# Performance work log

Hardware: AMD Instinct MI355X
Metric: run time of the kernel (lower is better)

The kernel has to match this reference:

```python
import jax, jax.numpy as jnp
import numpy as np

N_NODES = 100000
N_EDGES = 3200000
N_GRAPHS = 512
IN_DIM, HID, OUT, N_CLS = 32, 64, 64, 10


def _linear_params(key, din, dout, scale=0.05):
    k1, k2 = jax.random.split(key)
    return (jax.random.normal(k1, (din, dout), jnp.float32) * scale,
            jax.random.normal(k2, (dout,), jnp.float32) * scale)


def setup_inputs() -> dict:
    key = jax.random.key(0)
    ks = jax.random.split(key, 12)
    x = jax.random.normal(ks[0], (N_NODES, IN_DIM), jnp.float32)
    edge_index = jax.random.randint(ks[1], (2, N_EDGES), 0, N_NODES, jnp.int64)
    batch = jnp.sort(jax.random.randint(ks[2], (N_NODES,), 0, N_GRAPHS, jnp.int64))
    W_emb, b_emb = _linear_params(ks[3], IN_DIM, HID)
    W1, b1 = _linear_params(ks[4], HID, HID)
    W2, b2 = _linear_params(ks[5], HID, HID)
    W3, b3 = _linear_params(ks[6], HID, HID)
    W4, b4 = _linear_params(ks[7], HID, OUT)
    Wr1, br1 = _linear_params(ks[8], OUT, OUT // 2)
    Wr2, br2 = _linear_params(ks[9], OUT // 2, OUT // 4)
    Wr3, br3 = _linear_params(ks[10], OUT // 4, N_CLS)
    return dict(x=x, edge_index=edge_index, batch=batch, n_graphs=N_GRAPHS,
                W_emb=W_emb, b_emb=b_emb, W1=W1, b1=b1, W2=W2, b2=b2,
                W3=W3, b3=b3, W4=W4, b4=b4, Wr1=Wr1, br1=br1,
                Wr2=Wr2, br2=br2, Wr3=Wr3, br3=br3)


def reference(x, edge_index, batch, n_graphs,
              W_emb, b_emb, W1, b1, W2, b2, W3, b3, W4, b4,
              Wr1, br1, Wr2, br2, Wr3, br3):
    n = x.shape[0]
    # PyG GCNConv(normalize=True): add self-loops, symmetric D^{-1/2} norm
    self_idx = jnp.arange(n, dtype=edge_index.dtype)
    src = jnp.concatenate([edge_index[0], self_idx])  # [E+N]
    dst = jnp.concatenate([edge_index[1], self_idx])
    deg = jax.ops.segment_sum(jnp.ones(src.shape[0], x.dtype), dst, num_segments=n)
    dis = jnp.where(deg > 0, jax.lax.rsqrt(deg), 0.0)
    norm = dis[src] * dis[dst]  # [E+N]

    def gcn_conv(h, W, b):
        h = h @ W                              # [N, D]
        msg = h[src] * norm[:, None]           # gather + scale, [E+N, D]
        agg = jax.ops.segment_sum(msg, dst, num_segments=n)  # scatter-add
        return agg + b

    h = x @ W_emb + b_emb
    h = jax.nn.relu(gcn_conv(h, W1, b1))
    h = jax.nn.relu(gcn_conv(h, W2, b2))
    h = jax.nn.relu(gcn_conv(h, W3, b3))
    h = jax.nn.relu(gcn_conv(h, W4, b4))

    # global mean pool over graphs
    sums = jax.ops.segment_sum(h, batch, num_segments=n_graphs)
    cnts = jax.ops.segment_sum(jnp.ones(n, h.dtype), batch, num_segments=n_graphs)
    pooled = sums / jnp.maximum(cnts, 1.0)[:, None]

    r = jax.nn.relu(pooled @ Wr1 + br1)
    r = jax.nn.relu(r @ Wr2 + br2)
    logits = r @ Wr3 + br3
    return jax.nn.log_softmax(logits, axis=1)
```

## Files before the change

kernel.cpp:

```cpp
#include <hip/hip_runtime.h>
#include <hip/hip_bf16.h>

typedef __hip_bfloat16 bf16;
typedef short bf16x8 __attribute__((ext_vector_type(8)));
typedef float f32x4 __attribute__((ext_vector_type(4)));

#define N_NODES 100000
#define N_EDGES 3200000
#define N_GRAPHS 512
#define NBKT    ((N_NODES + 255) / 256)
#define CAP     10496
#define EPB     16384
#define NBLK_A  ((N_EDGES + EPB - 1) / EPB)
#define FP4_SCALE 16.0f
#define FP4_INV   (1.0f / 16.0f)


__device__ inline float fp8_to_f32(unsigned int b) {
    unsigned s = (b >> 7) & 1, e = (b >> 3) & 15, m = b & 7;
    float v = (e == 0) ? (float)m * 0.001953125f
                       : __uint_as_float(((e + 120u) << 23) | (m << 20));
    return s ? -v : v;
}

__device__ inline void acc4(float* a, unsigned v) {
#if __has_builtin(__builtin_amdgcn_cvt_pk_f32_fp8)
    typedef float f32x2 __attribute__((ext_vector_type(2)));
    f32x2 lo = __builtin_amdgcn_cvt_pk_f32_fp8((int)v, false);
    f32x2 hi = __builtin_amdgcn_cvt_pk_f32_fp8((int)v, true);
    a[0] += lo.x; a[1] += lo.y; a[2] += hi.x; a[3] += hi.y;
#elif __has_builtin(__builtin_amdgcn_cvt_f32_fp8)
    a[0] += __builtin_amdgcn_cvt_f32_fp8(v, 0);
    a[1] += __builtin_amdgcn_cvt_f32_fp8(v, 1);
    a[2] += __builtin_amdgcn_cvt_f32_fp8(v, 2);
    a[3] += __builtin_amdgcn_cvt_f32_fp8(v, 3);
#else
    a[0] += fp8_to_f32(v & 0xFF);
    a[1] += fp8_to_f32((v >> 8) & 0xFF);
    a[2] += fp8_to_f32((v >> 16) & 0xFF);
    a[3] += fp8_to_f32((v >> 24) & 0xFF);
#endif
}


__device__ inline void accf4(float* a, float* b, unsigned d) {
#if __has_builtin(__builtin_amdgcn_perm)
    unsigned lo8 = __builtin_amdgcn_perm(0x4C484440u, 0x3C383000u, d & 0x07070707u)
                 | ((d & 0x08080808u) << 4);
    unsigned hi8 = __builtin_amdgcn_perm(0x4C484440u, 0x3C383000u, (d >> 4) & 0x07070707u)
                 | (d & 0x80808080u);
#else
    unsigned lo8 = 0, hi8 = 0;
    #pragma unroll
    for (int i = 0; i < 4; ++i) {
        unsigned ln = (d >> (8 * i)) & 7u, hs_ = (d >> (8 * i)) & 0x80u;
        unsigned hn = (d >> (8 * i + 4)) & 7u, ls_ = ((d >> (8 * i)) & 8u) << 4;
        unsigned lb = (ln < 2) ? ln * 0x30u : (0x30u + (ln << 2));
        unsigned hb = (hn < 2) ? hn * 0x30u : (0x30u + (hn << 2));
        lo8 |= (lb | ls_) << (8 * i);
        hi8 |= (hb | hs_) << (8 * i);
    }
#endif
    acc4(a, lo8);
    acc4(b, hi8);
}


__device__ inline unsigned fp4n(float v) {
    unsigned s = (__float_as_uint(v) >> 28) & 8u;
    float x = fabsf(v);
    unsigned n = (unsigned)(x >= 0.25f) + (x >= 0.75f) + (x >= 1.25f) + (x >= 1.75f)
               + (x >= 2.5f) + (x >= 3.5f) + (x >= 5.0f);
    return s | n;
}

__device__ inline unsigned short f2bf(float x) {
    unsigned u = __float_as_uint(x);
    return (unsigned short)((u + 0x7FFF + ((u >> 16) & 1)) >> 16);
}


__global__ void k_setup(const float* __restrict__ W_emb, const float* __restrict__ b_emb,
                        const float* __restrict__ W1, const float* __restrict__ W2,
                        const float* __restrict__ W3, const float* __restrict__ W4,
                        float* __restrict__ Wc, float* __restrict__ bc,
                        unsigned short* __restrict__ Wfrag, int* __restrict__ gcur,
                        unsigned* __restrict__ ta, unsigned* __restrict__ tb) {
    int blk = blockIdx.x, t = threadIdx.x;
    if (blk == 0) {
        for (int i = t; i < 32 * 64; i += 256) {
            int a = i / 64, b = i % 64;
            float acc = 0.f;
            for (int k = 0; k < 64; ++k) acc += W_emb[a * 64 + k] * W1[k * 64 + b];
            Wc[i] = acc;
        }
        if (t < 64) {
            float acc = 0.f;
            for (int k = 0; k < 64; ++k) acc += b_emb[k] * W1[k * 64 + t];
            bc[t] = acc;
        }
    } else if (blk <= 3) {
        const float* W = (blk == 1) ? W2 : (blk == 2) ? W3 : W4;
        unsigned short* dst = Wfrag + (size_t)(blk - 1) * 4096;
        for (int i = 0; i < 16; ++i) {
            int flat = t * 16 + i;
            int j = flat & 7, lane = (flat >> 3) & 63, mt = (flat >> 9) & 3, kt = flat >> 11;
            int m = mt * 16 + (lane & 15);
            int k = kt * 32 + ((lane >> 4) << 3) + j;
            dst[flat] = f2bf(W[k * 64 + m]);
        }
    } else {
        for (int b = t; b < NBKT; b += 256) gcur[b] = b * CAP;
        if (t < 8) {
            size_t o = (size_t)N_NODES * 8 + t;
            ta[o] = 0; tb[o] = 0;
        }
    }
}


__global__ void __launch_bounds__(512) k_bucket(const int* __restrict__ ei,
                                                int* __restrict__ gcur,
                                                int* __restrict__ ebuf) {
    __shared__ int cnt[NBKT];
    __shared__ int base[NBKT];
    int t = threadIdx.x;
    for (int i = t; i < NBKT; i += 512) cnt[i] = 0;
    __syncthreads();
    int e0 = blockIdx.x * EPB + t;
    int sv[32], dv[32];
    #pragma unroll
    for (int j = 0; j < 32; ++j) {
        int e = e0 + j * 512;
        if (e < N_EDGES) {
            sv[j] = ei[e];
            dv[j] = ei[N_EDGES + e];
            atomicAdd(&cnt[dv[j] >> 8], 1);
        } else dv[j] = -1;
    }
    __syncthreads();
    for (int i = t; i < NBKT; i += 512) {
        base[i] = atomicAdd(&gcur[i], cnt[i]);
        cnt[i] = 0;
    }
    __syncthreads();
    #pragma unroll
    for (int j = 0; j < 32; ++j) {
        if (dv[j] >= 0) {
            int b = dv[j] >> 8;
            int r = atomicAdd(&cnt[b], 1);
            ebuf[base[b] + r] = (sv[j] << 8) | (dv[j] & 255);
        }
    }
}


__global__ void __launch_bounds__(256) k_fill2(const int* __restrict__ ebuf,
                                               const int* __restrict__ gcur,
                                               int2* __restrict__ rc,
                                               float* __restrict__ dis,
                                               int* __restrict__ col) {
    __shared__ int cnt[256];
    __shared__ int sc[256];
    __shared__ int exs[256];
    __shared__ int cur[256];
    int b = blockIdx.x, t = threadIdx.x;
    int n0 = b * 256;
    int nrec = gcur[b] - b * CAP;
    const int* eb = ebuf + (size_t)b * CAP;
    int* cw = col + (size_t)b * CAP;
    cnt[t] = 0; cur[t] = 0;
    __syncthreads();
    for (int i = t; i < nrec; i += 256)
        atomicAdd(&cnt[eb[i] & 255], 1);
    __syncthreads();
    int c0 = cnt[t];
    int a8 = (c0 + 7) & ~7;
    sc[t] = a8; __syncthreads();
    for (int off = 1; off < 256; off <<= 1) {
        int u = (t >= off) ? sc[t - off] : 0;
        __syncthreads();
        sc[t] += u;
        __syncthreads();
    }
    int myex = sc[t] - a8;
    exs[t] = myex;
    int n = n0 + t;
    if (n < N_NODES) {
        rc[n] = make_int2(b * CAP + myex, c0);
        dis[n] = rsqrtf((float)(c0 + 1));
    }
    for (int i = myex + c0; i < myex + a8; ++i) cw[i] = N_NODES;
    __syncthreads();
    for (int i = t; i < nrec; i += 256) {
        int rec = eb[i];
        int dl = rec & 255;
        cw[exs[dl] + atomicAdd(&cur[dl], 1)] = rec >> 8;
    }
}


__global__ void __launch_bounds__(256) k_mm1(const float* __restrict__ inp,
                                             const float* __restrict__ W,
                                             const float* __restrict__ bias,
                                             const float* __restrict__ dis,
                                             unsigned char* __restrict__ T) {
    __shared__ float Wl[32][64];
    __shared__ float hs[16][32];
    int t = threadIdx.x;
    for (int i = t; i < 32 * 64; i += 256) Wl[i / 64][i % 64] = W[i];
    int row0 = blockIdx.x * 16;
    for (int i = t; i < 16 * 32; i += 256) {
        int r = row0 + i / 32, k = i % 32;
        hs[i / 32][k] = inp[(size_t)r * 32 + k];
    }
    __syncthreads();
    int c = t & 63, rg = t >> 6;
    float a0 = 0, a1 = 0, a2 = 0, a3 = 0;
    #pragma unroll 4
    for (int k = 0; k < 32; ++k) {
        float wv = Wl[k][c];
        a0 += hs[rg * 4 + 0][k] * wv;
        a1 += hs[rg * 4 + 1][k] * wv;
        a2 += hs[rg * 4 + 2][k] * wv;
        a3 += hs[rg * 4 + 3][k] * wv;
    }
    float bv = bias[c];
    int r = row0 + rg * 4;
    unsigned n0 = fp4n(FP4_SCALE * dis[r + 0] * (a0 + bv));
    unsigned n1 = fp4n(FP4_SCALE * dis[r + 1] * (a1 + bv));
    unsigned n2 = fp4n(FP4_SCALE * dis[r + 2] * (a2 + bv));
    unsigned n3 = fp4n(FP4_SCALE * dis[r + 3] * (a3 + bv));
    unsigned p0 = __shfl_xor(n0, 1), p1 = __shfl_xor(n1, 1);
    unsigned p2 = __shfl_xor(n2, 1), p3 = __shfl_xor(n3, 1);
    if ((c & 1) == 0) {
        size_t boff = (size_t)(c >> 1);
        T[(size_t)(r + 0) * 32 + boff] = (unsigned char)(n0 | (p0 << 4));
        T[(size_t)(r + 1) * 32 + boff] = (unsigned char)(n1 | (p1 << 4));
        T[(size_t)(r + 2) * 32 + boff] = (unsigned char)(n2 | (p2 << 4));
        T[(size_t)(r + 3) * 32 + boff] = (unsigned char)(n3 | (p3 << 4));
    }
}


__global__ void __launch_bounds__(256, 8) k_agg(const unsigned* __restrict__ tph,
                                                const int2* __restrict__ rc,
                                                const int* __restrict__ col,
                                                unsigned short* __restrict__ agg) {
    int row = blockIdx.x * 32 + (threadIdx.x >> 3);
    int sl = threadIdx.x & 7;
    float a[4] = {0.f, 0.f, 0.f, 0.f};
    float b[4] = {0.f, 0.f, 0.f, 0.f};
    accf4(a, b, tph[(size_t)row * 8 + sl]);
    int2 r = rc[row];
    int nit = (r.y + 7) >> 3;
    const int* cp = col + r.x;
    if (nit > 0) {
        int4 c0 = *(const int4*)(cp + 0);
        int4 c1 = *(const int4*)(cp + 4);
        for (int it = 1; it < nit; ++it) {
            unsigned v0 = tph[(size_t)c0.x * 8 + sl];
            unsigned v1 = tph[(size_t)c0.y * 8 + sl];
            unsigned v2 = tph[(size_t)c0.z * 8 + sl];
            unsigned v3 = tph[(size_t)c0.w * 8 + sl];
            unsigned v4 = tph[(size_t)c1.x * 8 + sl];
            unsigned v5 = tph[(size_t)c1.y * 8 + sl];
            unsigned v6 = tph[(size_t)c1.z * 8 + sl];
            unsigned v7 = tph[(size_t)c1.w * 8 + sl];
            const int* np = cp + it * 8;
            c0 = *(const int4*)(np + 0);
            c1 = *(const int4*)(np + 4);
            accf4(a, b, v0); accf4(a, b, v1); accf4(a, b, v2); accf4(a, b, v3);
            accf4(a, b, v4); accf4(a, b, v5); accf4(a, b, v6); accf4(a, b, v7);
        }
        unsigned v0 = tph[(size_t)c0.x * 8 + sl];
        unsigned v1 = tph[(size_t)c0.y * 8 + sl];
        unsigned v2 = tph[(size_t)c0.z * 8 + sl];
        unsigned v3 = tph[(size_t)c0.w * 8 + sl];
        unsigned v4 = tph[(size_t)c1.x * 8 + sl];
        unsigned v5 = tph[(size_t)c1.y * 8 + sl];
        unsigned v6 = tph[(size_t)c1.z * 8 + sl];
        unsigned v7 = tph[(size_t)c1.w * 8 + sl];
        accf4(a, b, v0); accf4(a, b, v1); accf4(a, b, v2); accf4(a, b, v3);
        accf4(a, b, v4); accf4(a, b, v5); accf4(a, b, v6); accf4(a, b, v7);
    }
    uint4 o;
    o.x = (unsigned)f2bf(a[0]) | ((unsigned)f2bf(b[0]) << 16);
    o.y = (unsigned)f2bf(a[1]) | ((unsigned)f2bf(b[1]) << 16);
    o.z = (unsigned)f2bf(a[2]) | ((unsigned)f2bf(b[2]) << 16);
    o.w = (unsigned)f2bf(a[3]) | ((unsigned)f2bf(b[3]) << 16);
    *(uint4*)(agg + (size_t)row * 64 + sl * 8) = o;
}


__global__ void __launch_bounds__(256) k_combm(const unsigned short* __restrict__ agg,
                                               const float* __restrict__ dis,
                                               const float* __restrict__ bias,
                                               const unsigned short* __restrict__ Wfrag,
                                               unsigned char* __restrict__ T) {
    __shared__ unsigned short h_lds[64][72];
    int t = threadIdx.x;
    int rowbase = blockIdx.x * 64;
    {
        int row = t >> 2, q = t & 3;
        int grow = rowbase + row;
        if (grow < N_NODES) {
            float f = dis[grow] * FP4_INV;
            #pragma unroll
            for (int i = 0; i < 4; ++i) {
                int c0 = q * 16 + i * 4;
                ushort4 v = *(const ushort4*)(agg + (size_t)grow * 64 + c0);
                short4 o;
                o.x = (short)f2bf(fmaxf(f * __uint_as_float((unsigned)v.x << 16) + bias[c0 + 0], 0.f));
                o.y = (short)f2bf(fmaxf(f * __uint_as_float((unsigned)v.y << 16) + bias[c0 + 1], 0.f));
                o.z = (short)f2bf(fmaxf(f * __uint_as_float((unsigned)v.z << 16) + bias[c0 + 2], 0.f));
                o.w = (short)f2bf(fmaxf(f * __uint_as_float((unsigned)v.w << 16) + bias[c0 + 3], 0.f));
                *(short4*)&h_lds[row][c0] = o;
            }
        } else {
            #pragma unroll
            for (int i = 0; i < 4; ++i)
                *(short4*)&h_lds[row][q * 16 + i * 4] = make_short4(0, 0, 0, 0);
        }
    }
    __syncthreads();
    int w = t >> 6, l = t & 63;
    f32x4 acc[4] = {{0,0,0,0}, {0,0,0,0}, {0,0,0,0}, {0,0,0,0}};
    const bf16x8* wf = (const bf16x8*)Wfrag;
    #pragma unroll
    for (int kt = 0; kt < 2; ++kt) {
        bf16x8 bfr = *(const bf16x8*)&h_lds[w * 16 + (l & 15)][kt * 32 + ((l >> 4) << 3)];
        #pragma unroll
        for (int mt = 0; mt < 4; ++mt) {
            bf16x8 afr = wf[(kt * 4 + mt) * 64 + l];
            acc[mt] = __builtin_amdgcn_mfma_f32_16x16x32_bf16(afr, bfr, acc[mt], 0, 0, 0);
        }
    }
    int hrow = rowbase + w * 16 + (l & 15);
    if (hrow < N_NODES) {
        float sc2 = FP4_SCALE * dis[hrow];
        #pragma unroll
        for (int mt = 0; mt < 4; ++mt) {
            int colbase = mt * 16 + ((l >> 4) << 2);
            unsigned short v = (unsigned short)(fp4n(sc2 * acc[mt][0])
                               | (fp4n(sc2 * acc[mt][1]) << 4)
                               | (fp4n(sc2 * acc[mt][2]) << 8)
                               | (fp4n(sc2 * acc[mt][3]) << 12));
            *(unsigned short*)(T + (size_t)hrow * 32 + (colbase >> 1)) = v;
        }
    }
}


__global__ void __launch_bounds__(256) k_poolhead(const unsigned short* __restrict__ agg,
                                                  const float* __restrict__ dis,
                                                  const float* __restrict__ bias,
                                                  const int* __restrict__ batch,
                                                  const float* __restrict__ Wr1, const float* __restrict__ br1,
                                                  const float* __restrict__ Wr2, const float* __restrict__ br2,
                                                  const float* __restrict__ Wr3, const float* __restrict__ br3,
                                                  float* __restrict__ out) {
    __shared__ float part[4][64];
    __shared__ float p[64], r1[32], r2[16], lg[10];
    __shared__ int seg[2];
    int g = blockIdx.x, t = threadIdx.x;
    if (t < 2) {
        int key = g + t;
        int lo = 0, hi = N_NODES;
        while (lo < hi) { int m = (lo + hi) >> 1; if (batch[m] < key) lo = m + 1; else hi = m; }
        seg[t] = lo;
    }
    __syncthreads();
    int start = seg[0], end = seg[1];
    int w = t >> 6, grp = (t >> 4) & 3, sl = t & 15;
    float b0 = bias[sl * 4 + 0], b1 = bias[sl * 4 + 1];
    float b2 = bias[sl * 4 + 2], b3 = bias[sl * 4 + 3];
    float a[4] = {0.f, 0.f, 0.f, 0.f};
    for (int r = start + w * 4 + grp; r < end; r += 16) {
        ushort4 v = *(const ushort4*)(agg + (size_t)r * 64 + sl * 4);
        float s = dis[r] * FP4_INV;
        a[0] += fmaxf(s * __uint_as_float((unsigned)v.x << 16) + b0, 0.f);
        a[1] += fmaxf(s * __uint_as_float((unsigned)v.y << 16) + b1, 0.f);
        a[2] += fmaxf(s * __uint_as_float((unsigned)v.z << 16) + b2, 0.f);
        a[3] += fmaxf(s * __uint_as_float((unsigned)v.w << 16) + b3, 0.f);
    }
    #pragma unroll
    for (int j = 0; j < 4; ++j) {
        a[j] += __shfl_xor(a[j], 16);
        a[j] += __shfl_xor(a[j], 32);
    }
    if (sl == (t & 63)) {
        #pragma unroll
        for (int j = 0; j < 4; ++j) part[w][sl * 4 + j] = a[j];
    }
    __syncthreads();
    if (t < 64) {
        float s = part[0][t] + part[1][t] + part[2][t] + part[3][t];
        float c = fmaxf((float)(end - start), 1.f);
        p[t] = s / c;
    }
    __syncthreads();
    if (t < 32) {
        float acc = br1[t];
        for (int k = 0; k < 64; ++k) acc += p[k] * Wr1[k * 32 + t];
        r1[t] = fmaxf(acc, 0.f);
    }
    __syncthreads();
    if (t < 16) {
        float acc = br2[t];
        for (int k = 0; k < 32; ++k) acc += r1[k] * Wr2[k * 16 + t];
        r2[t] = fmaxf(acc, 0.f);
    }
    __syncthreads();
    if (t < 10) {
        float acc = br3[t];
        for (int k = 0; k < 16; ++k) acc += r2[k] * Wr3[k * 10 + t];
        lg[t] = acc;
    }
    __syncthreads();
    if (t < 10) {
        float m = -1e30f;
        for (int j = 0; j < 10; ++j) m = fmaxf(m, lg[j]);
        float s = 0.f;
        for (int j = 0; j < 10; ++j) s += expf(lg[j] - m);
        out[g * 10 + t] = lg[t] - m - logf(s);
    }
}

extern "C" void kernel_launch(void* const* d_in, const int* in_sizes, int n_in,
                              void* d_out, int out_size, void* d_ws, size_t ws_size,
                              hipStream_t stream) {
    const float* x     = (const float*)d_in[0];
    const int*   ei    = (const int*)d_in[1];
    const int*   batch = (const int*)d_in[2];
    const float* W_emb = (const float*)d_in[4];
    const float* b_emb = (const float*)d_in[5];
    const float* W1    = (const float*)d_in[6];
    const float* b1    = (const float*)d_in[7];
    const float* W2    = (const float*)d_in[8];
    const float* b2    = (const float*)d_in[9];
    const float* W3    = (const float*)d_in[10];
    const float* b3    = (const float*)d_in[11];
    const float* W4    = (const float*)d_in[12];
    const float* b4    = (const float*)d_in[13];
    const float* Wr1   = (const float*)d_in[14];
    const float* br1   = (const float*)d_in[15];
    const float* Wr2   = (const float*)d_in[16];
    const float* br2   = (const float*)d_in[17];
    const float* Wr3   = (const float*)d_in[18];
    const float* br3   = (const float*)d_in[19];
    float* out = (float*)d_out;

    char* ws = (char*)d_ws;
    size_t off = 0;
    auto alloc = [&](size_t b) { char* p = ws + off; off += (b + 511) & ~(size_t)511; return p; };
    size_t TBYTES = (size_t)(N_NODES + 1) * 32;
    int*   col    = (int*)  alloc((size_t)NBKT * CAP * 4);
    int*   ebuf   = (int*)  alloc((size_t)NBKT * CAP * 4);
    unsigned char* Ta = (unsigned char*)alloc(TBYTES);
    unsigned char* Tb = (unsigned char*)alloc(TBYTES);
    unsigned short* aggb = (unsigned short*)alloc((size_t)N_NODES * 64 * 2);
    int2*  rc     = (int2*) alloc((size_t)N_NODES * 8);
    float* dis    = (float*)alloc((size_t)N_NODES * 4);
    int*   gcur   = (int*)  alloc((size_t)NBKT * 4);
    float* Wc     = (float*)alloc(32 * 64 * 4);
    float* bc     = (float*)alloc(64 * 4);
    unsigned short* Wfrag = (unsigned short*)alloc(3 * 4096 * 2);

    k_setup<<<5, 256, 0, stream>>>(W_emb, b_emb, W1, W2, W3, W4, Wc, bc, Wfrag, gcur,
                                   (unsigned*)Ta, (unsigned*)Tb);
    k_bucket<<<NBLK_A, 512, 0, stream>>>(ei, gcur, ebuf);
    k_fill2<<<NBKT, 256, 0, stream>>>(ebuf, gcur, rc, dis, col);

    int nbm = N_NODES / 16;
    int nba = N_NODES / 32;
    int nbc = (N_NODES + 63) / 64;

    k_mm1<<<nbm, 256, 0, stream>>>(x, Wc, bc, dis, Ta);

    const float* lb[4] = {b1, b2, b3, b4};
    unsigned char* cur = Ta;
    unsigned char* nxt = Tb;
    for (int l = 0; l < 4; ++l) {
        k_agg<<<nba, 256, 0, stream>>>((const unsigned*)cur, rc, col, aggb);
        if (l < 3) {
            k_combm<<<nbc, 256, 0, stream>>>(aggb, dis, lb[l], Wfrag + (size_t)l * 4096, nxt);
            unsigned char* tmp = cur; cur = nxt; nxt = tmp;
        }
    }
    k_poolhead<<<N_GRAPHS, 256, 0, stream>>>(aggb, dis, b4, batch,
                                             Wr1, br1, Wr2, br2, Wr3, br3, out);
}
```

Before: 246.1 us.

## Fuse aggregation with combine MFMA and per-wave bucket counters

Merges the aggregation kernel with the following bias/ReLU/bf16 MFMA transform and fp4 quantization, so the bf16 aggregate buffer is no longer written and re-read between layers and three launches go away. The last layer applies bias and ReLU before writing, which simplifies the pooling kernel. The edge bucketing kernel now keeps per-wave shared counters to cut LDS atomic contention. FP4 decoding is rewritten to accumulate into packed float2 vectors. In exchange, each aggregation block now carries the MFMA tail and an LDS tile, which may raise register pressure in the gather loop.

```diff
diff --git a/kernel.cpp b/kernel.cpp
--- a/kernel.cpp
+++ b/kernel.cpp
@@ -4,6 +4,7 @@
 typedef __hip_bfloat16 bf16;
 typedef short bf16x8 __attribute__((ext_vector_type(8)));
 typedef float f32x4 __attribute__((ext_vector_type(4)));
+typedef float f32x2 __attribute__((ext_vector_type(2)));
 
 #define N_NODES 100000
 #define N_EDGES 3200000
@@ -23,46 +24,30 @@
     return s ? -v : v;
 }
 
-__device__ inline void acc4(float* a, unsigned v) {
-#if __has_builtin(__builtin_amdgcn_cvt_pk_f32_fp8)
-    typedef float f32x2 __attribute__((ext_vector_type(2)));
-    f32x2 lo = __builtin_amdgcn_cvt_pk_f32_fp8((int)v, false);
-    f32x2 hi = __builtin_amdgcn_cvt_pk_f32_fp8((int)v, true);
-    a[0] += lo.x; a[1] += lo.y; a[2] += hi.x; a[3] += hi.y;
-#elif __has_builtin(__builtin_amdgcn_cvt_f32_fp8)
-    a[0] += __builtin_amdgcn_cvt_f32_fp8(v, 0);
-    a[1] += __builtin_amdgcn_cvt_f32_fp8(v, 1);
-    a[2] += __builtin_amdgcn_cvt_f32_fp8(v, 2);
-    a[3] += __builtin_amdgcn_cvt_f32_fp8(v, 3);
-#else
-    a[0] += fp8_to_f32(v & 0xFF);
-    a[1] += fp8_to_f32((v >> 8) & 0xFF);
-    a[2] += fp8_to_f32((v >> 16) & 0xFF);
-    a[3] += fp8_to_f32((v >> 24) & 0xFF);
-#endif
-}
-
-
-__device__ inline void accf4(float* a, float* b, unsigned d) {
-#if __has_builtin(__builtin_amdgcn_perm)
+
+__device__ inline void accf4(f32x2* ae, f32x2* ao, unsigned d) {
+#if __has_builtin(__builtin_amdgcn_cvt_pk_f32_fp8) && __has_builtin(__builtin_amdgcn_perm)
     unsigned lo8 = __builtin_amdgcn_perm(0x4C484440u, 0x3C383000u, d & 0x07070707u)
                  | ((d & 0x08080808u) << 4);
     unsigned hi8 = __builtin_amdgcn_perm(0x4C484440u, 0x3C383000u, (d >> 4) & 0x07070707u)
                  | (d & 0x80808080u);
+    ae[0] += __builtin_amdgcn_cvt_pk_f32_fp8((int)lo8, false);
+    ae[1] += __builtin_amdgcn_cvt_pk_f32_fp8((int)lo8, true);
+    ao[0] += __builtin_amdgcn_cvt_pk_f32_fp8((int)hi8, false);
+    ao[1] += __builtin_amdgcn_cvt_pk_f32_fp8((int)hi8, true);
 #else
-    unsigned lo8 = 0, hi8 = 0;
     #pragma unroll
     for (int i = 0; i < 4; ++i) {
-        unsigned ln = (d >> (8 * i)) & 7u, hs_ = (d >> (8 * i)) & 0x80u;
-        unsigned hn = (d >> (8 * i + 4)) & 7u, ls_ = ((d >> (8 * i)) & 8u) << 4;
-        unsigned lb = (ln < 2) ? ln * 0x30u : (0x30u + (ln << 2));
-        unsigned hb = (hn < 2) ? hn * 0x30u : (0x30u + (hn << 2));
-        lo8 |= (lb | ls_) << (8 * i);
-        hi8 |= (hb | hs_) << (8 * i);
+        unsigned by = (d >> (8 * i)) & 0xFFu;
+        unsigned ln = by & 7u, hn = (by >> 4) & 7u;
+        float lv = (ln < 2) ? (float)ln * 0.5f : 0.5f * (float)(1 << ((ln >> 1) - 1)) * (2 + (ln & 1));
+        float hv = (hn < 2) ? (float)hn * 0.5f : 0.5f * (float)(1 << ((hn >> 1) - 1)) * (2 + (hn & 1));
+        if (by & 8u) lv = -lv;
+        if (by & 0x80u) hv = -hv;
+        ae[i >> 1][i & 1] += lv;
+        ao[i >> 1][i & 1] += hv;
     }
 #endif
-    acc4(a, lo8);
-    acc4(b, hi8);
 }
 
 
@@ -122,10 +107,10 @@
 __global__ void __launch_bounds__(512) k_bucket(const int* __restrict__ ei,
                                                 int* __restrict__ gcur,
                                                 int* __restrict__ ebuf) {
-    __shared__ int cnt[NBKT];
-    __shared__ int base[NBKT];
-    int t = threadIdx.x;
-    for (int i = t; i < NBKT; i += 512) cnt[i] = 0;
+    __shared__ int cnt[8][NBKT];
+    __shared__ int base[8][NBKT];
+    int t = threadIdx.x, w = t >> 6;
+    for (int i = t; i < 8 * NBKT; i += 512) ((int*)cnt)[i] = 0;
     __syncthreads();
     int e0 = blockIdx.x * EPB + t;
     int sv[32], dv[32];
@@ -135,21 +120,25 @@
         if (e < N_EDGES) {
             sv[j] = ei[e];
             dv[j] = ei[N_EDGES + e];
-            atomicAdd(&cnt[dv[j] >> 8], 1);
+            atomicAdd(&cnt[w][dv[j] >> 8], 1);
         } else dv[j] = -1;
     }
     __syncthreads();
-    for (int i = t; i < NBKT; i += 512) {
-        base[i] = atomicAdd(&gcur[i], cnt[i]);
-        cnt[i] = 0;
+    for (int b = t; b < NBKT; b += 512) {
+        int tot = 0, c[8];
+        #pragma unroll
+        for (int ww = 0; ww < 8; ++ww) { c[ww] = cnt[ww][b]; tot += c[ww]; }
+        int g = tot ? atomicAdd(&gcur[b], tot) : 0;
+        #pragma unroll
+        for (int ww = 0; ww < 8; ++ww) { base[ww][b] = g; g += c[ww]; cnt[ww][b] = 0; }
     }
     __syncthreads();
     #pragma unroll
     for (int j = 0; j < 32; ++j) {
         if (dv[j] >= 0) {
             int b = dv[j] >> 8;
-            int r = atomicAdd(&cnt[b], 1);
-            ebuf[base[b] + r] = (sv[j] << 8) | (dv[j] & 255);
+            int r = atomicAdd(&cnt[w][b], 1);
+            ebuf[base[w][b] + r] = (sv[j] << 8) | (dv[j] & 255);
         }
     }
 }
@@ -243,15 +232,23 @@
 }
 
 
-__global__ void __launch_bounds__(256, 8) k_agg(const unsigned* __restrict__ tph,
-                                                const int2* __restrict__ rc,
-                                                const int* __restrict__ col,
-                                                unsigned short* __restrict__ agg) {
-    int row = blockIdx.x * 32 + (threadIdx.x >> 3);
-    int sl = threadIdx.x & 7;
-    float a[4] = {0.f, 0.f, 0.f, 0.f};
-    float b[4] = {0.f, 0.f, 0.f, 0.f};
-    accf4(a, b, tph[(size_t)row * 8 + sl]);
+template<bool LAST>
+__global__ void __launch_bounds__(256, 8) k_aggc(const unsigned* __restrict__ tph,
+                                                 const int2* __restrict__ rc,
+                                                 const int* __restrict__ col,
+                                                 const float* __restrict__ dis,
+                                                 const float* __restrict__ bias,
+                                                 const unsigned short* __restrict__ Wfrag,
+                                                 unsigned char* __restrict__ Tn,
+                                                 unsigned short* __restrict__ hout) {
+    __shared__ unsigned short h_lds[32][72];
+    int t = threadIdx.x;
+    int rowbase = blockIdx.x * 32;
+    int row = rowbase + (t >> 3);
+    int sl = t & 7;
+    f32x2 ae[2] = {{0.f, 0.f}, {0.f, 0.f}};
+    f32x2 ao[2] = {{0.f, 0.f}, {0.f, 0.f}};
+    accf4(ae, ao, tph[(size_t)row * 8 + sl]);
     int2 r = rc[row];
     int nit = (r.y + 7) >> 3;
     const int* cp = col + r.x;
@@ -270,8 +267,8 @@
             const int* np = cp + it * 8;
             c0 = *(const int4*)(np + 0);
             c1 = *(const int4*)(np + 4);
-            accf4(a, b, v0); accf4(a, b, v1); accf4(a, b, v2); accf4(a, b, v3);
-            accf4(a, b, v4); accf4(a, b, v5); accf4(a, b, v6); accf4(a, b, v7);
+            accf4(ae, ao, v0); accf4(ae, ao, v1); accf4(ae, ao, v2); accf4(ae, ao, v3);
+            accf4(ae, ao, v4); accf4(ae, ao, v5); accf4(ae, ao, v6); accf4(ae, ao, v7);
         }
         unsigned v0 = tph[(size_t)c0.x * 8 + sl];
         unsigned v1 = tph[(size_t)c0.y * 8 + sl];
@@ -281,80 +278,58 @@
         unsigned v5 = tph[(size_t)c1.y * 8 + sl];
         unsigned v6 = tph[(size_t)c1.z * 8 + sl];
         unsigned v7 = tph[(size_t)c1.w * 8 + sl];
-        accf4(a, b, v0); accf4(a, b, v1); accf4(a, b, v2); accf4(a, b, v3);
-        accf4(a, b, v4); accf4(a, b, v5); accf4(a, b, v6); accf4(a, b, v7);
-    }
+        accf4(ae, ao, v0); accf4(ae, ao, v1); accf4(ae, ao, v2); accf4(ae, ao, v3);
+        accf4(ae, ao, v4); accf4(ae, ao, v5); accf4(ae, ao, v6); accf4(ae, ao, v7);
+    }
+    float ds = dis[row] * FP4_INV;
+    int f0 = sl * 8;
+    float h0 = fmaxf(ds * ae[0].x + bias[f0 + 0], 0.f);
+    float h1 = fmaxf(ds * ao[0].x + bias[f0 + 1], 0.f);
+    float h2 = fmaxf(ds * ae[0].y + bias[f0 + 2], 0.f);
+    float h3 = fmaxf(ds * ao[0].y + bias[f0 + 3], 0.f);
+    float h4 = fmaxf(ds * ae[1].x + bias[f0 + 4], 0.f);
+    float h5 = fmaxf(ds * ao[1].x + bias[f0 + 5], 0.f);
+    float h6 = fmaxf(ds * ae[1].y + bias[f0 + 6], 0.f);
+    float h7 = fmaxf(ds * ao[1].y + bias[f0 + 7], 0.f);
     uint4 o;
-    o.x = (unsigned)f2bf(a[0]) | ((unsigned)f2bf(b[0]) << 16);
-    o.y = (unsigned)f2bf(a[1]) | ((unsigned)f2bf(b[1]) << 16);
-    o.z = (unsigned)f2bf(a[2]) | ((unsigned)f2bf(b[2]) << 16);
-    o.w = (unsigned)f2bf(a[3]) | ((unsigned)f2bf(b[3]) << 16);
-    *(uint4*)(agg + (size_t)row * 64 + sl * 8) = o;
-}
-
-
-__global__ void __launch_bounds__(256) k_combm(const unsigned short* __restrict__ agg,
-                                               const float* __restrict__ dis,
-                                               const float* __restrict__ bias,
-                                               const unsigned short* __restrict__ Wfrag,
-                                               unsigned char* __restrict__ T) {
-    __shared__ unsigned short h_lds[64][72];
-    int t = threadIdx.x;
-    int rowbase = blockIdx.x * 64;
-    {
-        int row = t >> 2, q = t & 3;
-        int grow = rowbase + row;
-        if (grow < N_NODES) {
-            float f = dis[grow] * FP4_INV;
-            #pragma unroll
-            for (int i = 0; i < 4; ++i) {
-                int c0 = q * 16 + i * 4;
-                ushort4 v = *(const ushort4*)(agg + (size_t)grow * 64 + c0);
-                short4 o;
-                o.x = (short)f2bf(fmaxf(f * __uint_as_float((unsigned)v.x << 16) + bias[c0 + 0], 0.f));
-                o.y = (short)f2bf(fmaxf(f * __uint_as_float((unsigned)v.y << 16) + bias[c0 + 1], 0.f));
-                o.z = (short)f2bf(fmaxf(f * __uint_as_float((unsigned)v.z << 16) + bias[c0 + 2], 0.f));
-                o.w = (short)f2bf(fmaxf(f * __uint_as_float((unsigned)v.w << 16) + bias[c0 + 3], 0.f));
-                *(short4*)&h_lds[row][c0] = o;
-            }
-        } else {
-            #pragma unroll
-            for (int i = 0; i < 4; ++i)
-                *(short4*)&h_lds[row][q * 16 + i * 4] = make_short4(0, 0, 0, 0);
-        }
-    }
+    o.x = (unsigned)f2bf(h0) | ((unsigned)f2bf(h1) << 16);
+    o.y = (unsigned)f2bf(h2) | ((unsigned)f2bf(h3) << 16);
+    o.z = (unsigned)f2bf(h4) | ((unsigned)f2bf(h5) << 16);
+    o.w = (unsigned)f2bf(h6) | ((unsigned)f2bf(h7) << 16);
+    if (LAST) {
+        *(uint4*)(hout + (size_t)row * 64 + f0) = o;
+        return;
+    }
+    *(uint4*)&h_lds[row - rowbase][f0] = o;
     __syncthreads();
     int w = t >> 6, l = t & 63;
-    f32x4 acc[4] = {{0,0,0,0}, {0,0,0,0}, {0,0,0,0}, {0,0,0,0}};
+    int rg = w & 1, mt0 = (w >> 1) << 1;
+    f32x4 acc[2] = {{0, 0, 0, 0}, {0, 0, 0, 0}};
     const bf16x8* wf = (const bf16x8*)Wfrag;
     #pragma unroll
     for (int kt = 0; kt < 2; ++kt) {
-        bf16x8 bfr = *(const bf16x8*)&h_lds[w * 16 + (l & 15)][kt * 32 + ((l >> 4) << 3)];
+        bf16x8 bfr = *(const bf16x8*)&h_lds[rg * 16 + (l & 15)][kt * 32 + ((l >> 4) << 3)];
         #pragma unroll
-        for (int mt = 0; mt < 4; ++mt) {
-            bf16x8 afr = wf[(kt * 4 + mt) * 64 + l];
-            acc[mt] = __builtin_amdgcn_mfma_f32_16x16x32_bf16(afr, bfr, acc[mt], 0, 0, 0);
-        }
-    }
-    int hrow = rowbase + w * 16 + (l & 15);
-    if (hrow < N_NODES) {
-        float sc2 = FP4_SCALE * dis[hrow];
-        #pragma unroll
-        for (int mt = 0; mt < 4; ++mt) {
-            int colbase = mt * 16 + ((l >> 4) << 2);
-            unsigned short v = (unsigned short)(fp4n(sc2 * acc[mt][0])
-                               | (fp4n(sc2 * acc[mt][1]) << 4)
-                               | (fp4n(sc2 * acc[mt][2]) << 8)
-                               | (fp4n(sc2 * acc[mt][3]) << 12));
-            *(unsigned short*)(T + (size_t)hrow * 32 + (colbase >> 1)) = v;
-        }
-    }
-}
-
-
-__global__ void __launch_bounds__(256) k_poolhead(const unsigned short* __restrict__ agg,
-                                                  const float* __restrict__ dis,
-                                                  const float* __restrict__ bias,
+        for (int mi = 0; mi < 2; ++mi) {
+            bf16x8 afr = wf[(kt * 4 + mt0 + mi) * 64 + l];
+            acc[mi] = __builtin_amdgcn_mfma_f32_16x16x32_bf16(afr, bfr, acc[mi], 0, 0, 0);
+        }
+    }
+    int hrow = rowbase + rg * 16 + (l & 15);
+    float sc2 = FP4_SCALE * dis[hrow];
+    #pragma unroll
+    for (int mi = 0; mi < 2; ++mi) {
+        int colbase = (mt0 + mi) * 16 + ((l >> 4) << 2);
+        unsigned short v = (unsigned short)(fp4n(sc2 * acc[mi][0])
+                           | (fp4n(sc2 * acc[mi][1]) << 4)
+                           | (fp4n(sc2 * acc[mi][2]) << 8)
+                           | (fp4n(sc2 * acc[mi][3]) << 12));
+        *(unsigned short*)(Tn + (size_t)hrow * 32 + (colbase >> 1)) = v;
+    }
+}
+
+
+__global__ void __launch_bounds__(256) k_poolhead(const unsigned short* __restrict__ h,
                                                   const int* __restrict__ batch,
                                                   const float* __restrict__ Wr1, const float* __restrict__ br1,
                                                   const float* __restrict__ Wr2, const float* __restrict__ br2,
@@ -373,16 +348,13 @@
     __syncthreads();
     int start = seg[0], end = seg[1];
     int w = t >> 6, grp = (t >> 4) & 3, sl = t & 15;
-    float b0 = bias[sl * 4 + 0], b1 = bias[sl * 4 + 1];
-    float b2 = bias[sl * 4 + 2], b3 = bias[sl * 4 + 3];
     float a[4] = {0.f, 0.f, 0.f, 0.f};
     for (int r = start + w * 4 + grp; r < end; r += 16) {
-        ushort4 v = *(const ushort4*)(agg + (size_t)r * 64 + sl * 4);
-        float s = dis[r] * FP4_INV;
-        a[0] += fmaxf(s * __uint_as_float((unsigned)v.x << 16) + b0, 0.f);
-        a[1] += fmaxf(s * __uint_as_float((unsigned)v.y << 16) + b1, 0.f);
-        a[2] += fmaxf(s * __uint_as_float((unsigned)v.z << 16) + b2, 0.f);
-        a[3] += fmaxf(s * __uint_as_float((unsigned)v.w << 16) + b3, 0.f);
+        ushort4 v = *(const ushort4*)(h + (size_t)r * 64 + sl * 4);
+        a[0] += __uint_as_float((unsigned)v.x << 16);
+        a[1] += __uint_as_float((unsigned)v.y << 16);
+        a[2] += __uint_as_float((unsigned)v.z << 16);
+        a[3] += __uint_as_float((unsigned)v.w << 16);
     }
     #pragma unroll
     for (int j = 0; j < 4; ++j) {
@@ -459,7 +431,6 @@
     int*   ebuf   = (int*)  alloc((size_t)NBKT * CAP * 4);
     unsigned char* Ta = (unsigned char*)alloc(TBYTES);
     unsigned char* Tb = (unsigned char*)alloc(TBYTES);
-    unsigned short* aggb = (unsigned short*)alloc((size_t)N_NODES * 64 * 2);
     int2*  rc     = (int2*) alloc((size_t)N_NODES * 8);
     float* dis    = (float*)alloc((size_t)N_NODES * 4);
     int*   gcur   = (int*)  alloc((size_t)NBKT * 4);
@@ -467,6 +438,8 @@
     float* bc     = (float*)alloc(64 * 4);
     unsigned short* Wfrag = (unsigned short*)alloc(3 * 4096 * 2);
 
+    unsigned short* hout = (unsigned short*)ebuf;
+
     k_setup<<<5, 256, 0, stream>>>(W_emb, b_emb, W1, W2, W3, W4, Wc, bc, Wfrag, gcur,
                                    (unsigned*)Ta, (unsigned*)Tb);
     k_bucket<<<NBLK_A, 512, 0, stream>>>(ei, gcur, ebuf);
@@ -474,20 +447,17 @@
 
     int nbm = N_NODES / 16;
     int nba = N_NODES / 32;
-    int nbc = (N_NODES + 63) / 64;
 
     k_mm1<<<nbm, 256, 0, stream>>>(x, Wc, bc, dis, Ta);
 
-    const float* lb[4] = {b1, b2, b3, b4};
-    unsigned char* cur = Ta;
-    unsigned char* nxt = Tb;
-    for (int l = 0; l < 4; ++l) {
-        k_agg<<<nba, 256, 0, stream>>>((const unsigned*)cur, rc, col, aggb);
-        if (l < 3) {
-            k_combm<<<nbc, 256, 0, stream>>>(aggb, dis, lb[l], Wfrag + (size_t)l * 4096, nxt);
-            unsigned char* tmp = cur; cur = nxt; nxt = tmp;
-        }
-    }
-    k_poolhead<<<N_GRAPHS, 256, 0, stream>>>(aggb, dis, b4, batch,
-                                             Wr1, br1, Wr2, br2, Wr3, br3, out);
-}
+    k_aggc<false><<<nba, 256, 0, stream>>>((const unsigned*)Ta, rc, col, dis, b1,
+                                           Wfrag + 0 * 4096, Tb, nullptr);
+    k_aggc<false><<<nba, 256, 0, stream>>>((const unsigned*)Tb, rc, col, dis, b2,
+                                           Wfrag + 1 * 4096, Ta, nullptr);
+    k_aggc<false><<<nba, 256, 0, stream>>>((const unsigned*)Ta, rc, col, dis, b3,
+                                           Wfrag + 2 * 4096, Tb, nullptr);
+    k_aggc<true><<<nba, 256, 0, stream>>>((const unsigned*)Tb, rc, col, dis, b4,
+                                          nullptr, nullptr, hout);
+
+    k_poolhead<<<N_GRAPHS, 256, 0, stream>>>(hout, batch, Wr1, br1, Wr2, br2, Wr3, br3, out);
+}
```

After: 232.8 us. 1.06x faster.
